# Kernel tuning notes

Measured on AMD Instinct MI355X. Metric: run time of the kernel, lower is better.

Reference implementation:

```python
import math
import jax, jax.numpy as jnp
import numpy as np

B, C, D = 4, 2048, 1024
DQ = DV = 64
H = 16

def setup_inputs() -> dict:
    key = jax.random.key(0)
    kx, kq, kk, kv, kw = jax.random.split(key, 5)
    x = jax.random.normal(kx, (B, C, D), dtype=jnp.float32)
    # orthogonal-ish init: plain gaussians scaled so columns are ~unit norm
    Q = jax.random.normal(kq, (DQ, D, H), dtype=jnp.float32) / math.sqrt(D)
    K = jax.random.normal(kk, (DQ, D, H), dtype=jnp.float32) / math.sqrt(D)
    V = jax.random.normal(kv, (DV, D, H), dtype=jnp.float32) / math.sqrt(D)
    W = jax.random.normal(kw, (D, DV, H), dtype=jnp.float32) / math.sqrt(DV)
    return {"x": x, "Q": Q, "K": K, "V": V, "W": W}

def reference(x, Q, K, V, W):
    d_query, d_embed, num_heads = Q.shape
    d_value = V.shape[0]
    sq = math.sqrt(d_query / d_embed)
    sv = math.sqrt(d_value / d_embed)
    q = jnp.einsum('qdh,bcd->bhcq', Q, x) * sq            # [B,H,C,dq]
    k = jnp.einsum('qdh,bcd->bhcq', K, x) * sq            # [B,H,C,dq]
    v = jnp.einsum('vdh,bcd->bhcv', V, x) * sv            # [B,H,C,dv]
    att = jnp.einsum('bhcq,bhCq->bhcC', q, k) / d_query   # [B,H,C,C]
    T = x.shape[1]
    causal = jnp.arange(T)[:, None] >= jnp.arange(T)[None, :]  # lower-triangular
    att = jnp.where(causal, att, -jnp.inf)
    p = jax.nn.softmax(att, axis=-1)
    y = jnp.einsum('bhcC,bhCv->bhcv', p, v)               # [B,H,C,dv]
    z = jnp.einsum('dvh,bhcv->bcd', W, y) * (math.sqrt(d_embed / d_value) / num_heads)
    return z
```

## Files before the change

kernel.cpp:

```cpp
#include <hip/hip_runtime.h>
#include <hip/hip_bf16.h>

typedef __attribute__((ext_vector_type(8))) short bf16x8;
typedef __attribute__((ext_vector_type(4))) short s16x4;
typedef __attribute__((ext_vector_type(4))) float f32x4;
typedef __attribute__((ext_vector_type(2))) unsigned int u32x2;

#define AS1(p) ((const __attribute__((address_space(1))) void*)(p))
#define AS3(p) ((__attribute__((address_space(3))) void*)(p))
#define EXP2(x) __builtin_amdgcn_exp2f(x)

__device__ __forceinline__ unsigned short f2bf(float f) {
  __hip_bfloat16 h = __float2bfloat16(f);
  union { __hip_bfloat16 h; unsigned short s; } u; u.h = h; return u.s;
}
__device__ __forceinline__ unsigned pack2bf(float a, float b) {
  return ((unsigned)f2bf(b) << 16) | (unsigned)f2bf(a);
}

__device__ __forceinline__ f32x4 mfma16(s16x4 a, s16x4 b, f32x4 c) {
#if __has_builtin(__builtin_amdgcn_mfma_f32_16x16x16bf16_1k)
  return __builtin_amdgcn_mfma_f32_16x16x16bf16_1k(a, b, c, 0, 0, 0);
#else
  f32x4 d = c;
  asm volatile("v_mfma_f32_16x16x16_bf16 %0, %1, %2, %0" : "+v"(d) : "v"(a), "v"(b));
  return d;
#endif
}

__global__ void pack_wqkv(const float* __restrict__ Q, const float* __restrict__ K,
                          const float* __restrict__ V, short* __restrict__ WqkvT) {
  int idx = blockIdx.x * 256 + threadIdx.x;
  int sq = idx >> 12;
  int r = idx & 4095;
  int sel = sq >> 6, qd = sq & 63;
  const float* src = (sel == 0) ? Q : (sel == 1) ? K : V;
  float scale = (sel == 0) ? (0.03125f * 1.44269504f) : (sel == 1) ? 0.03125f : 0.25f;
  f32x4 v = *(const f32x4*)(src + (size_t)qd * 16384 + r * 4);
  int d = r >> 2, hb = (r & 3) * 4;
#pragma unroll
  for (int j = 0; j < 4; ++j)
    WqkvT[(size_t)(sel * 1024 + (hb + j) * 64 + qd) * 1024 + d] = (short)f2bf(v[j] * scale);
}

__global__ void pack_wo(const float* __restrict__ W, short* __restrict__ WoT) {
  int dcol = blockIdx.x;
  int t = threadIdx.x;
  f32x4 v = *(const f32x4*)(W + (size_t)dcol * 1024 + t * 4);
  int vd = t >> 2, hb = (t & 3) * 4;
#pragma unroll
  for (int j = 0; j < 4; ++j)
    WoT[(size_t)dcol * 1024 + (hb + j) * 64 + vd] = (short)f2bf(v[j] * 0.25f);
}

__global__ void pack_xk(const float* __restrict__ x, short* __restrict__ xb) {
  int i = blockIdx.x * 256 + threadIdx.x;
  if (i >= 2097152) return;
  f32x4 v = ((const f32x4*)x)[i];
  s16x4 o;
#pragma unroll
  for (int j = 0; j < 4; ++j) o[j] = (short)f2bf(v[j]);
  ((s16x4*)xb)[i] = o;
}

template <int MODE>
__global__ __launch_bounds__(256) void gemm_bt(const short* __restrict__ A,
                                               const short* __restrict__ Bt,
                                               void* __restrict__ Cout,
                                               int M, int N, int K) {
  __shared__ short As[128 * 64];
  __shared__ short Bs[128 * 64];
  const int tid = threadIdx.x;
  const int l = tid & 63, w = tid >> 6;
  const int g = l >> 4, lr = l & 15;
  const int m0 = blockIdx.y * 128, n0 = blockIdx.x * 128;
  const int wm = w >> 1, wn = w & 1;
  const int sr = l >> 3, sc = (l & 7) * 8;
  f32x4 acc[4][4] = {};
  for (int k0 = 0; k0 < K; k0 += 64) {
#pragma unroll
    for (int j = 0; j < 4; ++j) {
      int r0 = (w * 4 + j) * 8;
      __builtin_amdgcn_global_load_lds(AS1(A + (size_t)(m0 + r0 + sr) * K + k0 + sc),
                                       AS3(&As[r0 * 64]), 16, 0, 0);
      __builtin_amdgcn_global_load_lds(AS1(Bt + (size_t)(n0 + r0 + sr) * K + k0 + sc),
                                       AS3(&Bs[r0 * 64]), 16, 0, 0);
    }
    __syncthreads();
#pragma unroll
    for (int kc = 0; kc < 2; ++kc) {
      bf16x8 af[4], bfr[4];
#pragma unroll
      for (int i = 0; i < 4; ++i) {
        af[i]  = *(const bf16x8*)&As[(wm * 64 + i * 16 + lr) * 64 + kc * 32 + g * 8];
        bfr[i] = *(const bf16x8*)&Bs[(wn * 64 + i * 16 + lr) * 64 + kc * 32 + g * 8];
      }
#pragma unroll
      for (int mi = 0; mi < 4; ++mi)
#pragma unroll
        for (int ni = 0; ni < 4; ++ni)
          acc[mi][ni] = __builtin_amdgcn_mfma_f32_16x16x32_bf16(af[mi], bfr[ni], acc[mi][ni], 0, 0, 0);
    }
    __syncthreads();
  }
#pragma unroll
  for (int mi = 0; mi < 4; ++mi) {
#pragma unroll
    for (int ni = 0; ni < 4; ++ni) {
#pragma unroll
      for (int j = 0; j < 4; ++j) {
        int m = m0 + wm * 64 + mi * 16 + g * 4 + j;
        int n = n0 + wn * 64 + ni * 16 + lr;
        float val = acc[mi][ni][j];
        if (MODE == 0) {
          int sel = n >> 10, h = (n >> 6) & 15, qd = n & 63;
          int b = m >> 11, c = m & 2047;
          ((short*)Cout)[(size_t)sel * 8388608 + ((size_t)(b * 16 + h) * 2048 + c) * 64 + qd] =
              (short)f2bf(val);
        } else {
          ((float*)Cout)[(size_t)m * N + n] = val;
        }
      }
    }
  }
}

__global__ __launch_bounds__(256) void attn_fwd(const short* __restrict__ qkv,
                                                short* __restrict__ y2) {
  __shared__ short Ks[64 * 64];
  __shared__ short Vt[64 * 64];
  const int tid = threadIdx.x;
  const int l = tid & 63, w = tid >> 6;
  const int g = l >> 4, lr = l & 15;
  const int qbp = blockIdx.x;
  const int bh = blockIdx.y;
  const short* qp = qkv + (size_t)bh * 131072;
  const short* kp = qp + 8388608;
  const short* vp = qp + 16777216;
  const int b = bh >> 4, h = bh & 15;
  const int vkv0 = (tid >> 4) * 4;
  const int vvd4 = (tid & 15) * 4;
#pragma unroll 1
  for (int pass = 0; pass < 2; ++pass) {
    const int qb = pass ? (15 - qbp) : qbp;
    const int qw = qb * 128 + w * 32;
    bf16x8 qf[2][2];
#pragma unroll
    for (int qt = 0; qt < 2; ++qt)
#pragma unroll
      for (int kc = 0; kc < 2; ++kc)
        qf[qt][kc] = *(const bf16x8*)&qp[(qw + qt * 16 + lr) * 64 + kc * 32 + g * 8];
    float mrun[2] = {-__builtin_inff(), -__builtin_inff()};
    float lrun[2] = {0.f, 0.f};
    f32x4 acc[4][2] = {};
    const int nkv = qb * 2 + 2;
    for (int kvb = 0; kvb < nkv; ++kvb) {
      const int kv0 = kvb * 64;
#pragma unroll
      for (int j = 0; j < 2; ++j) {
        int r0 = (w * 2 + j) * 8;
        int r = r0 + (l >> 3);
        int sb = ((l & 7) * 16) ^ ((r & 7) << 4);
        __builtin_amdgcn_global_load_lds(AS1(kp + (size_t)(kv0 + r) * 64 + (sb >> 1)),
                                         AS3(&Ks[r0 * 64]), 16, 0, 0);
      }
      {
        const short* vrow = vp + (size_t)(kv0 + vkv0) * 64 + vvd4;
        s16x4 r0 = *(const s16x4*)(vrow);
        s16x4 r1 = *(const s16x4*)(vrow + 64);
        s16x4 r2 = *(const s16x4*)(vrow + 128);
        s16x4 r3 = *(const s16x4*)(vrow + 192);
        unsigned q0 = ((const unsigned*)&r0)[0], q1 = ((const unsigned*)&r0)[1];
        unsigned q2 = ((const unsigned*)&r1)[0], q3 = ((const unsigned*)&r1)[1];
        unsigned q4 = ((const unsigned*)&r2)[0], q5 = ((const unsigned*)&r2)[1];
        unsigned q6 = ((const unsigned*)&r3)[0], q7 = ((const unsigned*)&r3)[1];
#pragma unroll
        for (int c = 0; c < 4; ++c) {
          unsigned selb = (c & 1) ? 0x07060302u : 0x05040100u;
          unsigned lodw = (c < 2) ? __builtin_amdgcn_perm(q2, q0, selb)
                                  : __builtin_amdgcn_perm(q3, q1, selb);
          unsigned hidw = (c < 2) ? __builtin_amdgcn_perm(q6, q4, selb)
                                  : __builtin_amdgcn_perm(q7, q5, selb);
          int vd = vvd4 + c;
          int byte = vd * 128 + ((vkv0 * 2) ^ ((vd & 7) << 4));
          u32x2 wv; wv[0] = lodw; wv[1] = hidw;
          *(u32x2*)&Vt[byte >> 1] = wv;
        }
      }
      __syncthreads();
      if (kv0 <= qw + 31) {
        const bool needmask = (kv0 + 63 > qw);
        f32x4 st[4][2];
#pragma unroll
        for (int kt = 0; kt < 4; ++kt) {
          int r = kt * 16 + lr;
          int swz = (r & 7) << 4;
          bf16x8 kf0 = *(const bf16x8*)&Ks[(r * 128 + ((g * 16) ^ swz)) >> 1];
          bf16x8 kf1 = *(const bf16x8*)&Ks[(r * 128 + ((64 + g * 16) ^ swz)) >> 1];
#pragma unroll
          for (int qt = 0; qt < 2; ++qt) {
            f32x4 z = {0.f, 0.f, 0.f, 0.f};
            z = __builtin_amdgcn_mfma_f32_16x16x32_bf16(kf0, qf[qt][0], z, 0, 0, 0);
            z = __builtin_amdgcn_mfma_f32_16x16x32_bf16(kf1, qf[qt][1], z, 0, 0, 0);
            st[kt][qt] = z;
          }
        }
        if (needmask) {
#pragma unroll
          for (int kt = 0; kt < 4; ++kt)
#pragma unroll
            for (int qt = 0; qt < 2; ++qt)
#pragma unroll
              for (int i = 0; i < 4; ++i) {
                int kvg = kv0 + kt * 16 + g * 4 + i;
                int qg = qw + qt * 16 + lr;
                if (kvg > qg) st[kt][qt][i] = -__builtin_inff();
              }
        }
        unsigned pk[4][2][2];
#pragma unroll
        for (int qt = 0; qt < 2; ++qt) {
          float pm = -__builtin_inff();
#pragma unroll
          for (int kt = 0; kt < 4; ++kt)
#pragma unroll
            for (int i = 0; i < 4; ++i) pm = fmaxf(pm, st[kt][qt][i]);
          pm = fmaxf(pm, __shfl_xor(pm, 16));
          pm = fmaxf(pm, __shfl_xor(pm, 32));
          float mnew = fmaxf(mrun[qt], pm);
          float scale = EXP2(mrun[qt] - mnew);
          mrun[qt] = mnew;
          float rs = 0.f;
#pragma unroll
          for (int kt = 0; kt < 4; ++kt)
#pragma unroll
            for (int i = 0; i < 4; ++i) {
              float e = EXP2(st[kt][qt][i] - mnew);
              st[kt][qt][i] = e;
              rs += e;
            }
          rs += __shfl_xor(rs, 16);
          rs += __shfl_xor(rs, 32);
          lrun[qt] = lrun[qt] * scale + rs;
#pragma unroll
          for (int vt = 0; vt < 4; ++vt) acc[vt][qt] *= scale;
#pragma unroll
          for (int kt = 0; kt < 4; ++kt) {
            pk[kt][qt][0] = pack2bf(st[kt][qt][0], st[kt][qt][1]);
            pk[kt][qt][1] = pack2bf(st[kt][qt][2], st[kt][qt][3]);
          }
        }
#pragma unroll
        for (int kt = 0; kt < 4; ++kt) {
          s16x4 vf4[4];
#pragma unroll
          for (int vt = 0; vt < 4; ++vt) {
            int vd = vt * 16 + lr;
            vf4[vt] = *(const s16x4*)&Vt[(vd * 128 + ((kt * 32 + g * 8) ^ ((vd & 7) << 4))) >> 1];
          }
#pragma unroll
          for (int qt = 0; qt < 2; ++qt) {
            s16x4 pb;
            ((unsigned*)&pb)[0] = pk[kt][qt][0];
            ((unsigned*)&pb)[1] = pk[kt][qt][1];
#pragma unroll
            for (int vt = 0; vt < 4; ++vt)
              acc[vt][qt] = mfma16(vf4[vt], pb, acc[vt][qt]);
          }
        }
      }
      __syncthreads();
    }
#pragma unroll
    for (int qt = 0; qt < 2; ++qt) {
      float inv = 1.f / lrun[qt];
      int qg = qw + qt * 16 + lr;
#pragma unroll
      for (int vt = 0; vt < 4; ++vt) {
        s16x4 o;
#pragma unroll
        for (int j = 0; j < 4; ++j) o[j] = (short)f2bf(acc[vt][qt][j] * inv);
        *(s16x4*)&y2[((size_t)(b * 2048 + qg)) * 1024 + h * 64 + vt * 16 + g * 4] = o;
      }
    }
  }
}

extern "C" void kernel_launch(void* const* d_in, const int* in_sizes, int n_in,
                              void* d_out, int out_size, void* d_ws, size_t ws_size,
                              hipStream_t stream) {
  const float* x = (const float*)d_in[0];
  const float* Q = (const float*)d_in[1];
  const float* K = (const float*)d_in[2];
  const float* V = (const float*)d_in[3];
  const float* W = (const float*)d_in[4];
  char* ws = (char*)d_ws;
  short* WqkvT = (short*)ws;
  short* xb    = (short*)(ws + 6291456);
  short* qkv   = (short*)(ws + 23068672);
  short* WoT   = (short*)(ws + 73400320);
  short* y2    = xb;
  float* z     = (float*)d_out;

  pack_wqkv<<<3072, 256, 0, stream>>>(Q, K, V, WqkvT);
  pack_wo<<<1024, 256, 0, stream>>>(W, WoT);
  pack_xk<<<8192, 256, 0, stream>>>(x, xb);
  gemm_bt<0><<<dim3(24, 64), 256, 0, stream>>>(xb, WqkvT, (void*)qkv, 8192, 3072, 1024);
  attn_fwd<<<dim3(8, 64), 256, 0, stream>>>(qkv, y2);
  gemm_bt<1><<<dim3(8, 64), 256, 0, stream>>>(y2, WoT, (void*)z, 8192, 1024, 1024);
}
```

Measured before the change: 293.2 us.

## Halve attention query tile to 64 rows and add lazy softmax rescaling

The attention kernel now gives each wave 16 query rows instead of 32, so each block covers 64 queries. The grid doubles to 1024 flattened blocks, ordered so that blocks for different heads sit next to each other. Causal pairing is kept across 32 query blocks, and skipped KV tiles now track the finer causal edge more closely. The online softmax rescales the accumulator only when the new row max exceeds the running max by more than 8 (base-2 exponent units); this removes most rescaling work but lets unnormalized values grow before the final divide. In exchange, each K/V tile loaded into LDS is reused by half as many queries, so global and LDS traffic per unit of work roughly doubles.

After: 300.5 us. +2.5%, slower.

```diff
diff --git a/kernel.cpp b/kernel.cpp
--- a/kernel.cpp
+++ b/kernel.cpp
@@ -132,8 +132,9 @@
   const int tid = threadIdx.x;
   const int l = tid & 63, w = tid >> 6;
   const int g = l >> 4, lr = l & 15;
-  const int qbp = blockIdx.x;
-  const int bh = blockIdx.y;
+  const int wg = blockIdx.x;
+  const int qbp = wg >> 6;
+  const int bh = wg & 63;
   const short* qp = qkv + (size_t)bh * 131072;
   const short* kp = qp + 8388608;
   const short* vp = qp + 16777216;
@@ -142,18 +143,16 @@
   const int vvd4 = (tid & 15) * 4;
 #pragma unroll 1
   for (int pass = 0; pass < 2; ++pass) {
-    const int qb = pass ? (15 - qbp) : qbp;
-    const int qw = qb * 128 + w * 32;
-    bf16x8 qf[2][2];
-#pragma unroll
-    for (int qt = 0; qt < 2; ++qt)
-#pragma unroll
-      for (int kc = 0; kc < 2; ++kc)
-        qf[qt][kc] = *(const bf16x8*)&qp[(qw + qt * 16 + lr) * 64 + kc * 32 + g * 8];
-    float mrun[2] = {-__builtin_inff(), -__builtin_inff()};
-    float lrun[2] = {0.f, 0.f};
-    f32x4 acc[4][2] = {};
-    const int nkv = qb * 2 + 2;
+    const int qb = pass ? (31 - qbp) : qbp;
+    const int qw = qb * 64 + w * 16;
+    bf16x8 qf[2];
+#pragma unroll
+    for (int kc = 0; kc < 2; ++kc)
+      qf[kc] = *(const bf16x8*)&qp[(qw + lr) * 64 + kc * 32 + g * 8];
+    float mrun = -__builtin_inff();
+    float lrun = 0.f;
+    f32x4 acc[4] = {};
+    const int nkv = qb + 1;
     for (int kvb = 0; kvb < nkv; ++kvb) {
       const int kv0 = kvb * 64;
 #pragma unroll
@@ -188,100 +187,83 @@
         }
       }
       __syncthreads();
-      if (kv0 <= qw + 31) {
+      if (kv0 <= qw + 15) {
         const bool needmask = (kv0 + 63 > qw);
-        f32x4 st[4][2];
+        f32x4 st[4];
 #pragma unroll
         for (int kt = 0; kt < 4; ++kt) {
           int r = kt * 16 + lr;
           int swz = (r & 7) << 4;
           bf16x8 kf0 = *(const bf16x8*)&Ks[(r * 128 + ((g * 16) ^ swz)) >> 1];
           bf16x8 kf1 = *(const bf16x8*)&Ks[(r * 128 + ((64 + g * 16) ^ swz)) >> 1];
-#pragma unroll
-          for (int qt = 0; qt < 2; ++qt) {
-            f32x4 z = {0.f, 0.f, 0.f, 0.f};
-            z = __builtin_amdgcn_mfma_f32_16x16x32_bf16(kf0, qf[qt][0], z, 0, 0, 0);
-            z = __builtin_amdgcn_mfma_f32_16x16x32_bf16(kf1, qf[qt][1], z, 0, 0, 0);
-            st[kt][qt] = z;
+          f32x4 z = {0.f, 0.f, 0.f, 0.f};
+          z = __builtin_amdgcn_mfma_f32_16x16x32_bf16(kf0, qf[0], z, 0, 0, 0);
+          z = __builtin_amdgcn_mfma_f32_16x16x32_bf16(kf1, qf[1], z, 0, 0, 0);
+          st[kt] = z;
+        }
+        if (needmask) {
+#pragma unroll
+          for (int kt = 0; kt < 4; ++kt)
+#pragma unroll
+            for (int i = 0; i < 4; ++i) {
+              int kvg = kv0 + kt * 16 + g * 4 + i;
+              if (kvg > qw + lr) st[kt][i] = -__builtin_inff();
+            }
+        }
+        float pm = -__builtin_inff();
+#pragma unroll
+        for (int kt = 0; kt < 4; ++kt)
+#pragma unroll
+          for (int i = 0; i < 4; ++i) pm = fmaxf(pm, st[kt][i]);
+        pm = fmaxf(pm, __shfl_xor(pm, 16));
+        pm = fmaxf(pm, __shfl_xor(pm, 32));
+        if (!__all(pm <= mrun + 8.f)) {
+          float mnew = fmaxf(mrun, pm);
+          float scale = EXP2(mrun - mnew);
+          mrun = mnew;
+          lrun *= scale;
+#pragma unroll
+          for (int vt = 0; vt < 4; ++vt) acc[vt] *= scale;
+        }
+        float rs = 0.f;
+        unsigned pk[4][2];
+#pragma unroll
+        for (int kt = 0; kt < 4; ++kt) {
+#pragma unroll
+          for (int i = 0; i < 4; ++i) {
+            float e = EXP2(st[kt][i] - mrun);
+            st[kt][i] = e;
+            rs += e;
           }
-        }
-        if (needmask) {
-#pragma unroll
-          for (int kt = 0; kt < 4; ++kt)
-#pragma unroll
-            for (int qt = 0; qt < 2; ++qt)
-#pragma unroll
-              for (int i = 0; i < 4; ++i) {
-                int kvg = kv0 + kt * 16 + g * 4 + i;
-                int qg = qw + qt * 16 + lr;
-                if (kvg > qg) st[kt][qt][i] = -__builtin_inff();
-              }
-        }
-        unsigned pk[4][2][2];
-#pragma unroll
-        for (int qt = 0; qt < 2; ++qt) {
-          float pm = -__builtin_inff();
-#pragma unroll
-          for (int kt = 0; kt < 4; ++kt)
-#pragma unroll
-            for (int i = 0; i < 4; ++i) pm = fmaxf(pm, st[kt][qt][i]);
-          pm = fmaxf(pm, __shfl_xor(pm, 16));
-          pm = fmaxf(pm, __shfl_xor(pm, 32));
-          float mnew = fmaxf(mrun[qt], pm);
-          float scale = EXP2(mrun[qt] - mnew);
-          mrun[qt] = mnew;
-          float rs = 0.f;
-#pragma unroll
-          for (int kt = 0; kt < 4; ++kt)
-#pragma unroll
-            for (int i = 0; i < 4; ++i) {
-              float e = EXP2(st[kt][qt][i] - mnew);
-              st[kt][qt][i] = e;
-              rs += e;
-            }
-          rs += __shfl_xor(rs, 16);
-          rs += __shfl_xor(rs, 32);
-          lrun[qt] = lrun[qt] * scale + rs;
-#pragma unroll
-          for (int vt = 0; vt < 4; ++vt) acc[vt][qt] *= scale;
-#pragma unroll
-          for (int kt = 0; kt < 4; ++kt) {
-            pk[kt][qt][0] = pack2bf(st[kt][qt][0], st[kt][qt][1]);
-            pk[kt][qt][1] = pack2bf(st[kt][qt][2], st[kt][qt][3]);
-          }
-        }
+          pk[kt][0] = pack2bf(st[kt][0], st[kt][1]);
+          pk[kt][1] = pack2bf(st[kt][2], st[kt][3]);
+        }
+        rs += __shfl_xor(rs, 16);
+        rs += __shfl_xor(rs, 32);
+        lrun += rs;
 #pragma unroll
         for (int kt = 0; kt < 4; ++kt) {
-          s16x4 vf4[4];
+          s16x4 pb;
+          ((unsigned*)&pb)[0] = pk[kt][0];
+          ((unsigned*)&pb)[1] = pk[kt][1];
 #pragma unroll
           for (int vt = 0; vt < 4; ++vt) {
             int vd = vt * 16 + lr;
-            vf4[vt] = *(const s16x4*)&Vt[(vd * 128 + ((kt * 32 + g * 8) ^ ((vd & 7) << 4))) >> 1];
+            s16x4 vf4 = *(const s16x4*)&Vt[(vd * 128 + ((kt * 32 + g * 8) ^ ((vd & 7) << 4))) >> 1];
+            acc[vt] = mfma16(vf4, pb, acc[vt]);
           }
-#pragma unroll
-          for (int qt = 0; qt < 2; ++qt) {
-            s16x4 pb;
-            ((unsigned*)&pb)[0] = pk[kt][qt][0];
-            ((unsigned*)&pb)[1] = pk[kt][qt][1];
-#pragma unroll
-            for (int vt = 0; vt < 4; ++vt)
-              acc[vt][qt] = mfma16(vf4[vt], pb, acc[vt][qt]);
-          }
         }
       }
       __syncthreads();
     }
-#pragma unroll
-    for (int qt = 0; qt < 2; ++qt) {
-      float inv = 1.f / lrun[qt];
-      int qg = qw + qt * 16 + lr;
-#pragma unroll
-      for (int vt = 0; vt < 4; ++vt) {
-        s16x4 o;
-#pragma unroll
-        for (int j = 0; j < 4; ++j) o[j] = (short)f2bf(acc[vt][qt][j] * inv);
-        *(s16x4*)&y2[((size_t)(b * 2048 + qg)) * 1024 + h * 64 + vt * 16 + g * 4] = o;
-      }
+    float inv = 1.f / lrun;
+    int qg = qw + lr;
+#pragma unroll
+    for (int vt = 0; vt < 4; ++vt) {
+      s16x4 o;
+#pragma unroll
+      for (int j = 0; j < 4; ++j) o[j] = (short)f2bf(acc[vt][j] * inv);
+      *(s16x4*)&y2[((size_t)(b * 2048 + qg)) * 1024 + h * 64 + vt * 16 + g * 4] = o;
     }
   }
 }
@@ -306,6 +288,6 @@
   pack_wo<<<1024, 256, 0, stream>>>(W, WoT);
   pack_xk<<<8192, 256, 0, stream>>>(x, xb);
   gemm_bt<0><<<dim3(24, 64), 256, 0, stream>>>(xb, WqkvT, (void*)qkv, 8192, 3072, 1024);
-  attn_fwd<<<dim3(8, 64), 256, 0, stream>>>(qkv, y2);
+  attn_fwd<<<1024, 256, 0, stream>>>(qkv, y2);
   gemm_bt<1><<<dim3(8, 64), 256, 0, stream>>>(y2, WoT, (void*)z, 8192, 1024, 1024);
 }
```
